# Kernel optimization log

Measured on AMD Instinct MI355X. Metric: run time of the kernel, lower is better.

## Reference

```python
import jax, jax.numpy as jnp
import numpy as np


def setup_inputs() -> dict:
    key = jax.random.key(0)
    ks = jax.random.split(key, 8)
    B, C, H, W = 4, 512, 64, 64
    M = C // 8
    sq = 1.0 / np.sqrt(C)
    return {
        "x": jax.random.normal(ks[0], (B, C, H, W), jnp.float32),
        "Wq": jax.random.normal(ks[1], (M, C), jnp.float32) * sq,
        "bq": jnp.zeros((M,), jnp.float32),
        "Wk": jax.random.normal(ks[2], (M, C), jnp.float32) * sq,
        "bk": jnp.zeros((M,), jnp.float32),
        "Wv": jax.random.normal(ks[3], (C, C), jnp.float32) * sq,
        "bv": jnp.zeros((C,), jnp.float32),
        "gamma": jax.random.uniform(ks[4], (1,), jnp.float32),
    }


def reference(x, Wq, bq, Wk, bk, Wv, bv, gamma):
    B, C, H, W = x.shape
    N = H * W
    xf = x.reshape(B, C, N)  # flatten spatial -> [B, C, N]
    # 1x1 convs are channel-mixing matmuls
    q = jnp.einsum('mc,bcn->bmn', Wq, xf) + bq[None, :, None]  # [B, M, N]
    k = jnp.einsum('mc,bcn->bmn', Wk, xf) + bk[None, :, None]  # [B, M, N]
    v = jnp.einsum('dc,bcn->bdn', Wv, xf) + bv[None, :, None]  # [B, C, N]
    # sim[b,i,j] = <q[:, i], k[:, j]>, softmax over j
    sim = jnp.einsum('bmi,bmj->bij', q, k)  # [B, N, N]
    attn = jax.nn.softmax(sim, axis=-1)
    # feat[b,c,i] = sum_j v[b,c,j] * attn[b,i,j]
    feat = jnp.einsum('bcj,bij->bci', v, attn)  # [B, C, N]
    out = gamma[0] * feat.reshape(B, C, H, W) + x
    return out
```

## Files before the change

### kernel.cpp

```cpp
#include <hip/hip_runtime.h>

typedef _Float16 f16;
typedef _Float16 f16x8 __attribute__((ext_vector_type(8)));
typedef float    f32x4 __attribute__((ext_vector_type(4)));
typedef unsigned int u32x2 __attribute__((ext_vector_type(2)));

#define B_ 4
#define C_ 512
#define N_ 4096
#define M_ 64

__device__ __forceinline__ unsigned pk2(float a, float b) {
    union { f16 h[2]; unsigned u; } t;
    t.h[0] = (f16)a; t.h[1] = (f16)b;
    return t.u;
}

__global__ __launch_bounds__(256) void transpose_cast(
    const float* __restrict__ x, f16* __restrict__ xtf)
{
    __shared__ float sT[64][65];
    const int n0 = blockIdx.x * 64;
    const int c0 = blockIdx.y * 64;
    const int b  = blockIdx.z;
    const int tid = threadIdx.x;

    #pragma unroll
    for (int i = 0; i < 4; ++i) {
        int e = i * 256 + tid;
        int c = e >> 4;
        int n4 = (e & 15) * 4;
        float4 v = *(const float4*)(x + ((size_t)(b * C_ + c0 + c)) * N_ + n0 + n4);
        sT[c][n4 + 0] = v.x; sT[c][n4 + 1] = v.y;
        sT[c][n4 + 2] = v.z; sT[c][n4 + 3] = v.w;
    }
    __syncthreads();

    const int w = tid >> 6, lane = tid & 63, l15 = lane & 15, quad = lane >> 4;
    #pragma unroll
    for (int j = 0; j < 2; ++j) {
        const int fb  = w * 2 + j;
        const int lnt = fb >> 1, lck = fb & 1;
        const int nl  = lnt * 16 + l15;
        const int cb  = lck * 32 + quad * 8;
        f16x8 o;
        #pragma unroll
        for (int jj = 0; jj < 8; ++jj) o[jj] = (f16)sT[cb + jj][nl];
        const int ntg = (n0 >> 4) + lnt;
        const int ck  = (c0 >> 5) + lck;
        size_t idx = (((size_t)(b * 256 + ntg)) * 16 + ck) * 512 + lane * 8;
        *(f16x8*)(xtf + idx) = o;
    }
}

__global__ __launch_bounds__(512) void qkv_gemm(
    const f16* __restrict__ xtf,
    const float* __restrict__ Wq, const float* __restrict__ bq,
    const float* __restrict__ Wk, const float* __restrict__ bk,
    const float* __restrict__ Wv, const float* __restrict__ bv,
    f16* __restrict__ qt, f16* __restrict__ ktf, f16* __restrict__ vf)
{
    const int tid  = threadIdx.x;
    const int w    = tid >> 6;
    const int lane = tid & 63;
    const int l15  = lane & 15;
    const int quad = lane >> 4;
    const int nBase = blockIdx.x * 128;
    const int oseg  = blockIdx.y;
    const int b     = blockIdx.z;
    const int ot16  = w & 3;
    const int nhalf = w >> 2;

    const float* Wsel;
    if (oseg == 0)      Wsel = Wq;
    else if (oseg == 1) Wsel = Wk;
    else                Wsel = Wv + (size_t)(oseg - 2) * 64 * C_;

    const int orow = ot16 * 16 + l15;
    const float* wp = Wsel + (size_t)orow * C_ + quad * 8;

    const f16* xfb[4];
    #pragma unroll
    for (int ns = 0; ns < 4; ++ns) {
        int ntg = (nBase >> 4) + nhalf * 4 + ns;
        xfb[ns] = xtf + (((size_t)(b * 256 + ntg)) * 16) * 512 + lane * 8;
    }

    f32x4 acc[4] = {};

    float4 w0c = *(const float4*)(wp);
    float4 w1c = *(const float4*)(wp + 4);
    f16x8 b8c[4];
    #pragma unroll
    for (int ns = 0; ns < 4; ++ns) b8c[ns] = *(const f16x8*)(xfb[ns]);

    for (int ck = 0; ck < 16; ++ck) {
        float4 w0n, w1n;
        f16x8  b8n[4];
        if (ck + 1 < 16) {
            w0n = *(const float4*)(wp + ck * 32 + 32);
            w1n = *(const float4*)(wp + ck * 32 + 36);
            #pragma unroll
            for (int ns = 0; ns < 4; ++ns)
                b8n[ns] = *(const f16x8*)(xfb[ns] + (ck + 1) * 512);
        }
        f16x8 a8;
        a8[0]=(f16)w0c.x; a8[1]=(f16)w0c.y; a8[2]=(f16)w0c.z; a8[3]=(f16)w0c.w;
        a8[4]=(f16)w1c.x; a8[5]=(f16)w1c.y; a8[6]=(f16)w1c.z; a8[7]=(f16)w1c.w;
        #pragma unroll
        for (int ns = 0; ns < 4; ++ns)
            acc[ns] = __builtin_amdgcn_mfma_f32_16x16x32_f16(a8, b8c[ns], acc[ns], 0, 0, 0);
        w0c = w0n; w1c = w1n;
        #pragma unroll
        for (int ns = 0; ns < 4; ++ns) b8c[ns] = b8n[ns];
    }

    #pragma unroll
    for (int ns = 0; ns < 4; ++ns) {
        int n = nBase + nhalf * 64 + ns * 16 + l15;
        #pragma unroll
        for (int r = 0; r < 4; ++r) {
            int olocal = ot16 * 16 + quad * 4 + r;
            float bias;
            if (oseg == 0)      bias = bq[olocal];
            else if (oseg == 1) bias = bk[olocal];
            else                bias = bv[(oseg - 2) * 64 + olocal];
            f16 h = (f16)(acc[ns][r] + bias);
            if (oseg == 0) {
                qt[((size_t)(b * N_ + n)) * M_ + olocal] = h;
            } else if (oseg == 1) {
                size_t idx = (((size_t)b * 256 + (n >> 4)) * 2 + (olocal >> 5)) * 512
                           + (size_t)((((olocal >> 3) & 3) * 16 + (n & 15)) * 8) + (olocal & 7);
                ktf[idx] = h;
            } else {
                int c = (oseg - 2) * 64 + olocal;
                size_t idx = ((size_t)b * (C_ * N_)) + (size_t)(c >> 4) * 65536
                           + (size_t)(n >> 6) * 1024 + (size_t)((n >> 5) & 1) * 512
                           + (size_t)((((n >> 3) & 3) * 16 + (c & 15)) * 8) + (n & 7);
                vf[idx] = h;
            }
        }
    }
}

__global__ __launch_bounds__(512, 2) void attn(
    const f16* __restrict__ qt, const f16* __restrict__ ktf,
    const f16* __restrict__ vf, const float* __restrict__ x,
    const float* __restrict__ gamma, float* __restrict__ out)
{
    __shared__ __align__(16) char Pb[2][8192];
    __shared__ float mxs[8][4][16];
    __shared__ float lss[8][4][16];

    const int tid  = threadIdx.x;
    const int w    = tid >> 6;
    const int lane = tid & 63;
    const int l15  = lane & 15;
    const int quad = lane >> 4;
    const int jt   = w & 3;
    const int ish  = w >> 2;
    const int is0  = ish * 2, is1 = is0 + 1;

    const int lin  = blockIdx.x;
    const int b    = (lin & 7) >> 1;
    const int iblk = ((lin >> 3) << 1) | (lin & 1);
    const int i0   = iblk * 64;

    const f16* kln = ktf + (size_t)b * (N_ * M_) + lane * 8;
    const f16* vln = vf  + (size_t)b * (C_ * N_) + lane * 8;

    f16x8 bqf[4][2];
    #pragma unroll
    for (int is = 0; is < 4; ++is)
        #pragma unroll
        for (int kh = 0; kh < 2; ++kh)
            bqf[is][kh] = *(const f16x8*)(qt + ((size_t)(b * N_ + i0 + is * 16 + l15)) * M_
                                          + kh * 32 + quad * 8);

    float mx[4];
    #pragma unroll
    for (int is = 0; is < 4; ++is) mx[is] = -3.0e38f;
    {
        const f16* kw = kln + (size_t)(w * 512) * 64;
        f16x8 akc[4][2];
        #pragma unroll
        for (int t = 0; t < 4; ++t)
            #pragma unroll
            for (int kh = 0; kh < 2; ++kh)
                akc[t][kh] = *(const f16x8*)(kw + t * 1024 + kh * 512);

        #pragma unroll 2
        for (int jj = 0; jj < 512; jj += 64) {
            f16x8 akn[4][2];
            if (jj + 64 < 512) {
                const f16* kn = kw + (size_t)(jj + 64) * 64;
                #pragma unroll
                for (int t = 0; t < 4; ++t)
                    #pragma unroll
                    for (int kh = 0; kh < 2; ++kh)
                        akn[t][kh] = *(const f16x8*)(kn + t * 1024 + kh * 512);
            }
            #pragma unroll
            for (int t = 0; t < 4; ++t) {
                #pragma unroll
                for (int is = 0; is < 4; ++is) {
                    f32x4 s = {};
                    s = __builtin_amdgcn_mfma_f32_16x16x32_f16(akc[t][0], bqf[is][0], s, 0, 0, 0);
                    s = __builtin_amdgcn_mfma_f32_16x16x32_f16(akc[t][1], bqf[is][1], s, 0, 0, 0);
                    mx[is] = fmaxf(mx[is], fmaxf(fmaxf(s[0], s[1]), fmaxf(s[2], s[3])));
                }
            }
            #pragma unroll
            for (int t = 0; t < 4; ++t)
                #pragma unroll
                for (int kh = 0; kh < 2; ++kh)
                    akc[t][kh] = akn[t][kh];
        }
    }
    #pragma unroll
    for (int is = 0; is < 4; ++is) {
        mx[is] = fmaxf(mx[is], __shfl_xor(mx[is], 16, 64));
        mx[is] = fmaxf(mx[is], __shfl_xor(mx[is], 32, 64));
    }
    if (lane < 16) {
        #pragma unroll
        for (int is = 0; is < 4; ++is) mxs[w][is][lane] = mx[is];
    }
    __syncthreads();
    float m0 = -3.0e38f, m1 = -3.0e38f;
    #pragma unroll
    for (int w2 = 0; w2 < 8; ++w2) {
        m0 = fmaxf(m0, mxs[w2][is0][l15]);
        m1 = fmaxf(m1, mxs[w2][is1][l15]);
    }

    f32x4 acc[4][4] = {};
    float lp0 = 0.f, lp1 = 0.f;

    char* pbB = (char*)&Pb[0][0];
    const int swz = (l15 & 7) << 4;
    const int wb0 = ((is0 * 16 + l15) * 128 + (jt * 16 + quad * 4) * 2) ^ swz;
    const int wb1 = wb0 + 2048;
    int rb[4][2];
    #pragma unroll
    for (int is = 0; is < 4; ++is)
        #pragma unroll
        for (int kh = 0; kh < 2; ++kh)
            rb[is][kh] = ((is * 16 + l15) * 128 + kh * 64 + quad * 16) ^ swz;

    const f16* kp = kln + (size_t)(jt * 16) * 64;
    f16x8 ak0 = *(const f16x8*)(kp);
    f16x8 ak1 = *(const f16x8*)(kp + 512);
    const int cw = w * 4;
    int buf = 0;

    for (int j0 = 0; j0 < N_; j0 += 64) {
        const f16* vt = vln + (size_t)(j0 >> 6) * 1024;
        f16x8 vb0[4];
        #pragma unroll
        for (int ct = 0; ct < 4; ++ct)
            vb0[ct] = *(const f16x8*)(vt + (size_t)(cw + ct) * 65536);

        f32x4 s0 = {}, s1 = {};
        s0 = __builtin_amdgcn_mfma_f32_16x16x32_f16(ak0, bqf[is0][0], s0, 0, 0, 0);
        s0 = __builtin_amdgcn_mfma_f32_16x16x32_f16(ak1, bqf[is0][1], s0, 0, 0, 0);
        s1 = __builtin_amdgcn_mfma_f32_16x16x32_f16(ak0, bqf[is1][0], s1, 0, 0, 0);
        s1 = __builtin_amdgcn_mfma_f32_16x16x32_f16(ak1, bqf[is1][1], s1, 0, 0, 0);

        f16x8 akn0 = ak0, akn1 = ak1;
        if (j0 + 64 < N_) {
            const f16* kn = kp + (size_t)(j0 + 64) * 64;
            akn0 = *(const f16x8*)(kn);
            akn1 = *(const f16x8*)(kn + 512);
        }

        {
            float p0 = __expf(s0[0] - m0), p1 = __expf(s0[1] - m0);
            float p2 = __expf(s0[2] - m0), p3 = __expf(s0[3] - m0);
            lp0 += (p0 + p1) + (p2 + p3);
            u32x2 pw = { pk2(p0, p1), pk2(p2, p3) };
            *(u32x2*)(pbB + buf * 8192 + wb0) = pw;
        }
        {
            float q0 = __expf(s1[0] - m1), q1 = __expf(s1[1] - m1);
            float q2 = __expf(s1[2] - m1), q3 = __expf(s1[3] - m1);
            lp1 += (q0 + q1) + (q2 + q3);
            u32x2 pw = { pk2(q0, q1), pk2(q2, q3) };
            *(u32x2*)(pbB + buf * 8192 + wb1) = pw;
        }

        f16x8 vb1[4];
        #pragma unroll
        for (int ct = 0; ct < 4; ++ct)
            vb1[ct] = *(const f16x8*)(vt + (size_t)(cw + ct) * 65536 + 512);

        __syncthreads();

        f16x8 pbf[4][2];
        #pragma unroll
        for (int is = 0; is < 4; ++is)
            #pragma unroll
            for (int kh = 0; kh < 2; ++kh)
                pbf[is][kh] = *(const f16x8*)(pbB + buf * 8192 + rb[is][kh]);

        __builtin_amdgcn_s_setprio(1);
        #pragma unroll
        for (int ct = 0; ct < 4; ++ct)
            #pragma unroll
            for (int is = 0; is < 4; ++is)
                acc[ct][is] = __builtin_amdgcn_mfma_f32_16x16x32_f16(vb0[ct], pbf[is][0], acc[ct][is], 0, 0, 0);
        #pragma unroll
        for (int ct = 0; ct < 4; ++ct)
            #pragma unroll
            for (int is = 0; is < 4; ++is)
                acc[ct][is] = __builtin_amdgcn_mfma_f32_16x16x32_f16(vb1[ct], pbf[is][1], acc[ct][is], 0, 0, 0);
        __builtin_amdgcn_s_setprio(0);

        ak0 = akn0; ak1 = akn1;
        buf ^= 1;
    }

    lp0 += __shfl_xor(lp0, 16, 64);
    lp0 += __shfl_xor(lp0, 32, 64);
    lp1 += __shfl_xor(lp1, 16, 64);
    lp1 += __shfl_xor(lp1, 32, 64);
    if (lane < 16) { lss[w][is0][lane] = lp0; lss[w][is1][lane] = lp1; }
    __syncthreads();

    float linv[4];
    #pragma unroll
    for (int is = 0; is < 4; ++is) {
        const int wb = (is >> 1) * 4;
        float l = (lss[wb + 0][is][l15] + lss[wb + 1][is][l15])
                + (lss[wb + 2][is][l15] + lss[wb + 3][is][l15]);
        linv[is] = 1.0f / l;
    }

    const float g = gamma[0];
    #pragma unroll
    for (int is = 0; is < 4; ++is) {
        const int i = i0 + is * 16 + l15;
        #pragma unroll
        for (int ct = 0; ct < 4; ++ct) {
            #pragma unroll
            for (int r = 0; r < 4; ++r) {
                const int c = w * 64 + ct * 16 + quad * 4 + r;
                const size_t idx = ((size_t)(b * C_ + c)) * N_ + i;
                out[idx] = g * (acc[ct][is][r] * linv[is]) + x[idx];
            }
        }
    }
}

extern "C" void kernel_launch(void* const* d_in, const int* in_sizes, int n_in,
                              void* d_out, int out_size, void* d_ws, size_t ws_size,
                              hipStream_t stream)
{
    const float* x     = (const float*)d_in[0];
    const float* Wq    = (const float*)d_in[1];
    const float* bq    = (const float*)d_in[2];
    const float* Wk    = (const float*)d_in[3];
    const float* bk    = (const float*)d_in[4];
    const float* Wv    = (const float*)d_in[5];
    const float* bv    = (const float*)d_in[6];
    const float* gamma = (const float*)d_in[7];
    float* out = (float*)d_out;

    char* ws = (char*)d_ws;
    f16* xtf = (f16*)ws;
    f16* qt  = (f16*)(ws + (size_t)B_ * N_ * C_ * 2);
    f16* ktf = qt + (size_t)B_ * N_ * M_;
    f16* vf  = ktf + (size_t)B_ * N_ * M_;

    transpose_cast<<<dim3(N_ / 64, C_ / 64, B_), 256, 0, stream>>>(x, xtf);
    qkv_gemm<<<dim3(N_ / 128, 10, B_), 512, 0, stream>>>(
        xtf, Wq, bq, Wk, bk, Wv, bv, qt, ktf, vf);
    attn<<<dim3(256), 512, 0, stream>>>(qt, ktf, vf, x, gamma, out);
}
```

Measured before the change: 262.7 us.

## Software-pipeline attention loop: compute next P tile while accumulating current PV

Restructures the main attention loop into a prologue, steady state and epilogue. Each iteration computes QK^T and the exp for tile t+1 and writes it to the alternate LDS buffer while the PV MFMAs consume tile t, with V and K registers prefetched one tile ahead. This leaves one barrier per iteration that no longer sits between the P write and its read. The goal is to hide the exp/LDS latency and the global loads behind the MFMA work, at the cost of more live registers (vc/vn double buffers).

```diff
diff --git a/kernel.cpp b/kernel.cpp
--- a/kernel.cpp
+++ b/kernel.cpp
@@ -249,29 +249,65 @@
             rb[is][kh] = ((is * 16 + l15) * 128 + kh * 64 + quad * 16) ^ swz;
 
     const f16* kp = kln + (size_t)(jt * 16) * 64;
+    const int cw = w * 4;
+
     f16x8 ak0 = *(const f16x8*)(kp);
     f16x8 ak1 = *(const f16x8*)(kp + 512);
-    const int cw = w * 4;
-    int buf = 0;
-
-    for (int j0 = 0; j0 < N_; j0 += 64) {
-        const f16* vt = vln + (size_t)(j0 >> 6) * 1024;
-        f16x8 vb0[4];
-        #pragma unroll
-        for (int ct = 0; ct < 4; ++ct)
-            vb0[ct] = *(const f16x8*)(vt + (size_t)(cw + ct) * 65536);
-
+    {
         f32x4 s0 = {}, s1 = {};
         s0 = __builtin_amdgcn_mfma_f32_16x16x32_f16(ak0, bqf[is0][0], s0, 0, 0, 0);
         s0 = __builtin_amdgcn_mfma_f32_16x16x32_f16(ak1, bqf[is0][1], s0, 0, 0, 0);
         s1 = __builtin_amdgcn_mfma_f32_16x16x32_f16(ak0, bqf[is1][0], s1, 0, 0, 0);
         s1 = __builtin_amdgcn_mfma_f32_16x16x32_f16(ak1, bqf[is1][1], s1, 0, 0, 0);
-
-        f16x8 akn0 = ak0, akn1 = ak1;
-        if (j0 + 64 < N_) {
-            const f16* kn = kp + (size_t)(j0 + 64) * 64;
-            akn0 = *(const f16x8*)(kn);
-            akn1 = *(const f16x8*)(kn + 512);
+        float p0 = __expf(s0[0] - m0), p1 = __expf(s0[1] - m0);
+        float p2 = __expf(s0[2] - m0), p3 = __expf(s0[3] - m0);
+        lp0 += (p0 + p1) + (p2 + p3);
+        u32x2 pw0 = { pk2(p0, p1), pk2(p2, p3) };
+        *(u32x2*)(pbB + wb0) = pw0;
+        float q0 = __expf(s1[0] - m1), q1 = __expf(s1[1] - m1);
+        float q2 = __expf(s1[2] - m1), q3 = __expf(s1[3] - m1);
+        lp1 += (q0 + q1) + (q2 + q3);
+        u32x2 pw1 = { pk2(q0, q1), pk2(q2, q3) };
+        *(u32x2*)(pbB + wb1) = pw1;
+    }
+    ak0 = *(const f16x8*)(kp + 4096);
+    ak1 = *(const f16x8*)(kp + 4096 + 512);
+    f16x8 vc0[4], vc1[4];
+    #pragma unroll
+    for (int ct = 0; ct < 4; ++ct) {
+        vc0[ct] = *(const f16x8*)(vln + (size_t)(cw + ct) * 65536);
+        vc1[ct] = *(const f16x8*)(vln + (size_t)(cw + ct) * 65536 + 512);
+    }
+    __syncthreads();
+
+    #pragma unroll 2
+    for (int t = 0; t < 63; ++t) {
+        const int cb = (t & 1) * 8192;
+        const int nb = ((t + 1) & 1) * 8192;
+
+        f16x8 pbf[4][2];
+        #pragma unroll
+        for (int is = 0; is < 4; ++is)
+            #pragma unroll
+            for (int kh = 0; kh < 2; ++kh)
+                pbf[is][kh] = *(const f16x8*)(pbB + cb + rb[is][kh]);
+
+        f32x4 s0 = {}, s1 = {};
+        s0 = __builtin_amdgcn_mfma_f32_16x16x32_f16(ak0, bqf[is0][0], s0, 0, 0, 0);
+        s0 = __builtin_amdgcn_mfma_f32_16x16x32_f16(ak1, bqf[is0][1], s0, 0, 0, 0);
+        s1 = __builtin_amdgcn_mfma_f32_16x16x32_f16(ak0, bqf[is1][0], s1, 0, 0, 0);
+        s1 = __builtin_amdgcn_mfma_f32_16x16x32_f16(ak1, bqf[is1][1], s1, 0, 0, 0);
+
+        if (t + 2 < 64) {
+            ak0 = *(const f16x8*)(kp + (size_t)(t + 2) * 4096);
+            ak1 = *(const f16x8*)(kp + (size_t)(t + 2) * 4096 + 512);
+        }
+        const f16* vt = vln + (size_t)(t + 1) * 1024;
+        f16x8 vn0[4], vn1[4];
+        #pragma unroll
+        for (int ct = 0; ct < 4; ++ct) {
+            vn0[ct] = *(const f16x8*)(vt + (size_t)(cw + ct) * 65536);
+            vn1[ct] = *(const f16x8*)(vt + (size_t)(cw + ct) * 65536 + 512);
         }
 
         {
@@ -279,45 +315,53 @@
             float p2 = __expf(s0[2] - m0), p3 = __expf(s0[3] - m0);
             lp0 += (p0 + p1) + (p2 + p3);
             u32x2 pw = { pk2(p0, p1), pk2(p2, p3) };
-            *(u32x2*)(pbB + buf * 8192 + wb0) = pw;
+            *(u32x2*)(pbB + nb + wb0) = pw;
         }
         {
             float q0 = __expf(s1[0] - m1), q1 = __expf(s1[1] - m1);
             float q2 = __expf(s1[2] - m1), q3 = __expf(s1[3] - m1);
             lp1 += (q0 + q1) + (q2 + q3);
             u32x2 pw = { pk2(q0, q1), pk2(q2, q3) };
-            *(u32x2*)(pbB + buf * 8192 + wb1) = pw;
-        }
-
-        f16x8 vb1[4];
+            *(u32x2*)(pbB + nb + wb1) = pw;
+        }
+
+        __builtin_amdgcn_s_setprio(1);
         #pragma unroll
         for (int ct = 0; ct < 4; ++ct)
-            vb1[ct] = *(const f16x8*)(vt + (size_t)(cw + ct) * 65536 + 512);
+            #pragma unroll
+            for (int is = 0; is < 4; ++is)
+                acc[ct][is] = __builtin_amdgcn_mfma_f32_16x16x32_f16(vc0[ct], pbf[is][0], acc[ct][is], 0, 0, 0);
+        #pragma unroll
+        for (int ct = 0; ct < 4; ++ct)
+            #pragma unroll
+            for (int is = 0; is < 4; ++is)
+                acc[ct][is] = __builtin_amdgcn_mfma_f32_16x16x32_f16(vc1[ct], pbf[is][1], acc[ct][is], 0, 0, 0);
+        __builtin_amdgcn_s_setprio(0);
 
         __syncthreads();
 
+        #pragma unroll
+        for (int ct = 0; ct < 4; ++ct) { vc0[ct] = vn0[ct]; vc1[ct] = vn1[ct]; }
+    }
+
+    {
+        const int cb = (63 & 1) * 8192;
         f16x8 pbf[4][2];
         #pragma unroll
         for (int is = 0; is < 4; ++is)
             #pragma unroll
             for (int kh = 0; kh < 2; ++kh)
-                pbf[is][kh] = *(const f16x8*)(pbB + buf * 8192 + rb[is][kh]);
-
-        __builtin_amdgcn_s_setprio(1);
+                pbf[is][kh] = *(const f16x8*)(pbB + cb + rb[is][kh]);
         #pragma unroll
         for (int ct = 0; ct < 4; ++ct)
             #pragma unroll
             for (int is = 0; is < 4; ++is)
-                acc[ct][is] = __builtin_amdgcn_mfma_f32_16x16x32_f16(vb0[ct], pbf[is][0], acc[ct][is], 0, 0, 0);
+                acc[ct][is] = __builtin_amdgcn_mfma_f32_16x16x32_f16(vc0[ct], pbf[is][0], acc[ct][is], 0, 0, 0);
         #pragma unroll
         for (int ct = 0; ct < 4; ++ct)
             #pragma unroll
             for (int is = 0; is < 4; ++is)
-                acc[ct][is] = __builtin_amdgcn_mfma_f32_16x16x32_f16(vb1[ct], pbf[is][1], acc[ct][is], 0, 0, 0);
-        __builtin_amdgcn_s_setprio(0);
-
-        ak0 = akn0; ak1 = akn1;
-        buf ^= 1;
+                acc[ct][is] = __builtin_amdgcn_mfma_f32_16x16x32_f16(vc1[ct], pbf[is][1], acc[ct][is], 0, 0, 0);
     }
 
     lp0 += __shfl_xor(lp0, 16, 64);
```

After: 259.2 us. Within noise of the previous version (-1.3%).
